# Kernel tuning notes

Hardware: AMD Instinct MI355X
Metric: run time of the kernel (lower is better)

The kernel has to match this reference:

```python
import jax, jax.numpy as jnp
import numpy as np

N_NODES = 100000
N_EDGES = 1600000
IN_DIM = 128
HID = 64
N_CLASSES = 40
NEG_SLOPE = 0.2


def setup_inputs() -> dict:
    key = jax.random.key(0)
    ks = jax.random.split(key, 12)
    s_in = 1.0 / np.sqrt(IN_DIM)
    s_h = 1.0 / np.sqrt(HID)
    return {
        "x": jax.random.normal(ks[0], (N_NODES, IN_DIM), dtype=jnp.float32),
        "edge_index": jax.random.randint(ks[1], (2, N_EDGES), 0, N_NODES, dtype=jnp.int64),
        "W0": jax.random.normal(ks[2], (IN_DIM, HID), dtype=jnp.float32) * s_in,
        "a_s0": jax.random.normal(ks[3], (HID,), dtype=jnp.float32) * s_h,
        "a_d0": jax.random.normal(ks[4], (HID,), dtype=jnp.float32) * s_h,
        "b0": jnp.zeros((HID,), dtype=jnp.float32),
        "W1": jax.random.normal(ks[5], (HID, HID), dtype=jnp.float32) * s_h,
        "a_s1": jax.random.normal(ks[6], (HID,), dtype=jnp.float32) * s_h,
        "a_d1": jax.random.normal(ks[7], (HID,), dtype=jnp.float32) * s_h,
        "b1": jnp.zeros((HID,), dtype=jnp.float32),
        "Wl": jax.random.normal(ks[8], (HID, N_CLASSES), dtype=jnp.float32) * s_h,
        "bl": jnp.zeros((N_CLASSES,), dtype=jnp.float32),
    }


def gat_conv(x, src, dst, W, a_s, a_d, b, n_nodes):
    # single-head GATConv (PyG default heads=1), self-loops already in src/dst
    h = x @ W                                  # [N, d]
    e = jax.nn.leaky_relu((h @ a_s)[src] + (h @ a_d)[dst], NEG_SLOPE)  # [E]
    # segment softmax over incoming edges of each dst node
    m = jax.ops.segment_max(e, dst, num_segments=n_nodes)
    p = jnp.exp(e - m[dst])
    denom = jax.ops.segment_sum(p, dst, num_segments=n_nodes)
    alpha = p / (denom[dst] + 1e-16)           # [E]
    out = jax.ops.segment_sum(alpha[:, None] * h[src], dst, num_segments=n_nodes)
    return out + b


def reference(x, edge_index, W0, a_s0, a_d0, b0, W1, a_s1, a_d1, b1, Wl, bl):
    n = x.shape[0]
    loop = jnp.arange(n, dtype=edge_index.dtype)
    src = jnp.concatenate([edge_index[0], loop])
    dst = jnp.concatenate([edge_index[1], loop])
    h = gat_conv(x, src, dst, W0, a_s0, a_d0, b0, n)
    h = jax.nn.elu(h)
    h = gat_conv(h, src, dst, W1, a_s1, a_d1, b1, n)
    h = jax.nn.elu(h)
    return h @ Wl + bl
```

## Files before the change

### kernel.cpp

```cpp
#include <hip/hip_runtime.h>
#include <math.h>

#define NEG_SLOPE 0.2f
#define CAP 256
#define BSH 9
#define BSZ 512
#define CHUNK 2048
#define PADS 16
#define HGRID 256

typedef __attribute__((ext_vector_type(8))) short short8;
typedef __attribute__((ext_vector_type(4))) float f32x4;

__device__ __forceinline__ float hred_sum(float v) {
#pragma unroll
    for (int o = 16; o >= 1; o >>= 1) v += __shfl_xor(v, o, 64);
    return v;
}
__device__ __forceinline__ unsigned int f2bf(float f) {
    unsigned int u = __float_as_uint(f);
    return (u + 0x7fffu + ((u >> 16) & 1u)) >> 16;
}
__device__ __forceinline__ float bflo(unsigned int u) { return __uint_as_float(u << 16); }
__device__ __forceinline__ float bfhi(unsigned int u) { return __uint_as_float(u & 0xffff0000u); }


__global__ __launch_bounds__(256) void k_hist(const int* __restrict__ dst, int* __restrict__ bpart, int E) {
    __shared__ int lh[256];
    lh[threadIdx.x] = 0;
    __syncthreads();
    int gid = blockIdx.x * 256 + threadIdx.x;
    int nth = gridDim.x * 256;
    int E4 = E >> 2;
    for (int i = gid; i < E4; i += nth) {
        int4 d = ((const int4*)dst)[i];
        atomicAdd(&lh[d.x >> BSH], 1);
        atomicAdd(&lh[d.y >> BSH], 1);
        atomicAdd(&lh[d.z >> BSH], 1);
        atomicAdd(&lh[d.w >> BSH], 1);
    }
    for (int i = (E4 << 2) + gid; i < E; i += nth)
        atomicAdd(&lh[dst[i] >> BSH], 1);
    __syncthreads();
    bpart[blockIdx.x * 256 + threadIdx.x] = lh[threadIdx.x];
}

__global__ __launch_bounds__(256) void k_bscan(const int* __restrict__ bpart,
                                               int* __restrict__ eoff, int* __restrict__ boff,
                                               int* __restrict__ bcursor, int* __restrict__ ecnt,
                                               int* __restrict__ rowptr,
                                               int nbuck, int N, int E) {
    __shared__ int s1[256], s2[256];
    int t = threadIdx.x;
    int bc = 0;
    for (int b = 0; b < HGRID; b += 4) {
        bc += bpart[(b + 0) * 256 + t];
        bc += bpart[(b + 1) * 256 + t];
        bc += bpart[(b + 2) * 256 + t];
        bc += bpart[(b + 3) * 256 + t];
    }
    if (t >= nbuck) bc = 0;
    int cn = 0;
    if (t < nbuck) { cn = N - (t << BSH); if (cn > BSZ) cn = BSZ; if (cn < 0) cn = 0; }
    int tot = bc + cn;
    s1[t] = bc; s2[t] = tot;
    __syncthreads();
#pragma unroll
    for (int off = 1; off < 256; off <<= 1) {
        int u1 = (t >= off) ? s1[t - off] : 0;
        int u2 = (t >= off) ? s2[t - off] : 0;
        __syncthreads();
        s1[t] += u1; s2[t] += u2;
        __syncthreads();
    }
    if (t < nbuck) {
        int e = s1[t] - bc, b = s2[t] - tot;
        eoff[t] = e; boff[t] = b; ecnt[t] = bc; bcursor[t * PADS] = e;
    }
    if (t == 0) rowptr[N] = E + N;
}


__device__ __forceinline__ void scatter_body(char* smem, int bid,
        const int* __restrict__ src, const int* __restrict__ dst,
        int* __restrict__ bcursor, int* __restrict__ ebuf, int E) {
    int* lh = (int*)smem;
    int* lb = lh + 256;
    const int tid = threadIdx.x;
    int base = bid * CHUNK;
    int sv[8], dv[8];
    bool ok[8];
#pragma unroll
    for (int u = 0; u < 8; ++u) {
        int i = base + u * 256 + tid;
        ok[u] = i < E;
        int ii = ok[u] ? i : E - 1;
        dv[u] = dst[ii];
        sv[u] = src[ii];
    }
    lh[tid] = 0;
    __syncthreads();
#pragma unroll
    for (int u = 0; u < 8; ++u)
        if (ok[u]) atomicAdd(&lh[dv[u] >> BSH], 1);
    __syncthreads();
    int c = lh[tid];
    lb[tid] = c ? atomicAdd(&bcursor[tid * PADS], c) : 0;
    lh[tid] = 0;
    __syncthreads();
#pragma unroll
    for (int u = 0; u < 8; ++u) {
        if (ok[u]) {
            int d = dv[u], b = d >> BSH;
            int pp = atomicAdd(&lh[b], 1);
            ebuf[lb[b] + pp] = (sv[u] << BSH) | (d & (BSZ - 1));
        }
    }
}

__device__ __forceinline__ void gemm0_body(char* smem, int bid,
        const float* __restrict__ X, const float* __restrict__ W,
        const float* __restrict__ a_s, const float* __restrict__ a_d,
        unsigned int* __restrict__ hb, float* __restrict__ ss, float* __restrict__ sd, int N) {
    constexpr int K = 128, OUTW = 64, NKC = K / 32, NC = OUTW / 16;
    short* wfrag = (short*)smem;
    unsigned int* hs = (unsigned int*)(smem + NKC * NC * 64 * 8 * 2);

    const int tid  = threadIdx.x;
    const int lane = tid & 63;
    const int w    = tid >> 6;
    const int m    = lane & 15;
    const int q8   = lane >> 4;
    const int rowbase = bid * 64 + w * 16;

    for (int f = tid; f < NKC * NC * 64; f += 256) {
        int flane = f & 63;
        int fc    = (f >> 6) % NC;
        int fkc   = (f >> 6) / NC;
        int col   = fc * 16 + (flane & 15);
        int k0    = fkc * 32 + (flane >> 4) * 8;
        short8 b;
#pragma unroll
        for (int j = 0; j < 8; ++j) b[j] = (short)f2bf(W[(k0 + j) * OUTW + col]);
        *(short8*)&wfrag[f * 8] = b;
    }
    __syncthreads();

    int grow = rowbase + m; if (grow >= N) grow = N - 1;

    f32x4 acc[NC];
#pragma unroll
    for (int c = 0; c < NC; ++c) acc[c] = (f32x4)0.f;

    const float* xrow = X + (size_t)grow * K + q8 * 8;
#pragma unroll
    for (int kc = 0; kc < NKC; ++kc) {
        float4 v0 = *(const float4*)(xrow + kc * 32);
        float4 v1 = *(const float4*)(xrow + kc * 32 + 4);
        float vv[8] = {v0.x, v0.y, v0.z, v0.w, v1.x, v1.y, v1.z, v1.w};
        short8 ah, al;
#pragma unroll
        for (int j = 0; j < 8; ++j) {
            unsigned int hb16 = f2bf(vv[j]);
            ah[j] = (short)hb16;
            al[j] = (short)f2bf(vv[j] - __uint_as_float(hb16 << 16));
        }
#pragma unroll
        for (int c = 0; c < NC; ++c) {
            short8 b = *(short8*)&wfrag[((kc * NC + c) * 64 + lane) * 8];
            acc[c] = __builtin_amdgcn_mfma_f32_16x16x32_bf16(ah, b, acc[c], 0, 0, 0);
            acc[c] = __builtin_amdgcn_mfma_f32_16x16x32_bf16(al, b, acc[c], 0, 0, 0);
        }
    }

    float asv[NC], adv[NC];
#pragma unroll
    for (int c = 0; c < NC; ++c) { asv[c] = a_s[c * 16 + m]; adv[c] = a_d[c * 16 + m]; }
#pragma unroll
    for (int i = 0; i < 4; ++i) {
        float s = 0.f, d = 0.f;
#pragma unroll
        for (int c = 0; c < NC; ++c) {
            s = fmaf(acc[c][i], asv[c], s);
            d = fmaf(acc[c][i], adv[c], d);
        }
#pragma unroll
        for (int o = 1; o <= 8; o <<= 1) {
            s += __shfl_xor(s, o, 64);
            d += __shfl_xor(d, o, 64);
        }
        int r = rowbase + q8 * 4 + i;
        if (m == 0 && r < N) { ss[r] = s; sd[r] = d; }
    }

    unsigned short* hsw = (unsigned short*)&hs[w * 512];
#pragma unroll
    for (int c = 0; c < NC; ++c)
#pragma unroll
        for (int i = 0; i < 4; ++i)
            hsw[(q8 * 4 + i) * 64 + c * 16 + m] = (unsigned short)f2bf(acc[c][i]);
    unsigned int* hu = &hs[w * 512];
    int row = lane >> 2, u0 = (lane & 3) * 8;
    uint4 va = *(uint4*)&hu[row * 32 + u0];
    uint4 vb = *(uint4*)&hu[row * 32 + u0 + 4];
    int r = rowbase + row;
    if (r < N) {
        *(uint4*)&hb[(size_t)r * 32 + u0]     = va;
        *(uint4*)&hb[(size_t)r * 32 + u0 + 4] = vb;
    }
}

__global__ __launch_bounds__(256) void k_scatter_gemm0(
        const int* __restrict__ src, const int* __restrict__ dst,
        int* __restrict__ bcursor, int* __restrict__ ebuf, int E, int nscat,
        const float* __restrict__ X, const float* __restrict__ W,
        const float* __restrict__ a_s, const float* __restrict__ a_d,
        unsigned int* __restrict__ hb, float* __restrict__ ss, float* __restrict__ sd, int N) {
    __shared__ __align__(16) char smem[24576];
    if ((int)blockIdx.x < nscat)
        scatter_body(smem, blockIdx.x, src, dst, bcursor, ebuf, E);
    else
        gemm0_body(smem, blockIdx.x - nscat, X, W, a_s, a_d, hb, ss, sd, N);
}

__global__ __launch_bounds__(512) void k_build(const int* __restrict__ eoff, const int* __restrict__ boff,
                                               const int* __restrict__ ecnt, const int* __restrict__ ebuf,
                                               int* __restrict__ rowptr, int* __restrict__ csr, int N) {
    __shared__ int sdeg[BSZ], sscan[BSZ];
    int b = blockIdx.x, t = threadIdx.x;
    int nlo = b << BSH;
    int cn = N - nlo; if (cn > BSZ) cn = BSZ;
    int e0 = eoff[b], ec = ecnt[b], cb = boff[b];
    sdeg[t] = (t < cn) ? 1 : 0;
    __syncthreads();
    {
        int i = t;
        for (; i + 1536 < ec; i += 2048) {
            int r0 = ebuf[e0 + i], r1 = ebuf[e0 + i + 512];
            int r2 = ebuf[e0 + i + 1024], r3 = ebuf[e0 + i + 1536];
            atomicAdd(&sdeg[r0 & (BSZ - 1)], 1);
            atomicAdd(&sdeg[r1 & (BSZ - 1)], 1);
            atomicAdd(&sdeg[r2 & (BSZ - 1)], 1);
            atomicAdd(&sdeg[r3 & (BSZ - 1)], 1);
        }
        for (; i < ec; i += 512)
            atomicAdd(&sdeg[ebuf[e0 + i] & (BSZ - 1)], 1);
    }
    __syncthreads();
    int v = sdeg[t];
    sscan[t] = v;
    __syncthreads();
#pragma unroll
    for (int off = 1; off < BSZ; off <<= 1) {
        int u = (t >= off) ? sscan[t - off] : 0;
        __syncthreads();
        sscan[t] += u;
        __syncthreads();
    }
    int excl = sscan[t] - v;
    if (t < cn) {
        rowptr[nlo + t] = cb + excl;
        csr[cb + excl] = nlo + t;
        sdeg[t] = excl + 1;
    }
    __syncthreads();
    {
        int i = t;
        for (; i + 1536 < ec; i += 2048) {
            int r0 = ebuf[e0 + i], r1 = ebuf[e0 + i + 512];
            int r2 = ebuf[e0 + i + 1024], r3 = ebuf[e0 + i + 1536];
            int p0 = atomicAdd(&sdeg[r0 & (BSZ - 1)], 1);
            int p1 = atomicAdd(&sdeg[r1 & (BSZ - 1)], 1);
            int p2 = atomicAdd(&sdeg[r2 & (BSZ - 1)], 1);
            int p3 = atomicAdd(&sdeg[r3 & (BSZ - 1)], 1);
            csr[cb + p0] = r0 >> BSH;
            csr[cb + p1] = r1 >> BSH;
            csr[cb + p2] = r2 >> BSH;
            csr[cb + p3] = r3 >> BSH;
        }
        for (; i < ec; i += 512) {
            int rec = ebuf[e0 + i];
            int p = atomicAdd(&sdeg[rec & (BSZ - 1)], 1);
            csr[cb + p] = rec >> BSH;
        }
    }
}


template <int K, int OUTW, bool SS, bool HB, bool XB>
__global__ __launch_bounds__(256) void k_gemm(const void* __restrict__ X,
                                              const float* __restrict__ W,
                                              const float* __restrict__ a_s,
                                              const float* __restrict__ a_d,
                                              const float* __restrict__ bias,
                                              void* __restrict__ Hout,
                                              float* __restrict__ ss,
                                              float* __restrict__ sd, int N) {
    constexpr int NKC = K / 32;
    constexpr int NC  = (OUTW + 15) / 16;
    __shared__ __align__(16) short wfrag[NKC * NC * 64 * 8];
    __shared__ __align__(16) unsigned int hs[HB ? 4 : 1][16 * 32];

    const int tid  = threadIdx.x;
    const int lane = tid & 63;
    const int w    = tid >> 6;
    const int m    = lane & 15;
    const int q8   = lane >> 4;
    const int rowbase = blockIdx.x * 64 + w * 16;

    for (int f = tid; f < NKC * NC * 64; f += 256) {
        int flane = f & 63;
        int fc    = (f >> 6) % NC;
        int fkc   = (f >> 6) / NC;
        int col   = fc * 16 + (flane & 15);
        int k0    = fkc * 32 + (flane >> 4) * 8;
        short8 b;
#pragma unroll
        for (int j = 0; j < 8; ++j) {
            float v = (col < OUTW) ? W[(k0 + j) * OUTW + col] : 0.f;
            b[j] = (short)f2bf(v);
        }
        *(short8*)&wfrag[f * 8] = b;
    }
    __syncthreads();

    int grow = rowbase + m; if (grow >= N) grow = N - 1;

    f32x4 acc[NC];
#pragma unroll
    for (int c = 0; c < NC; ++c) acc[c] = (f32x4)0.f;

    if (XB) {
        const unsigned short* xrow = (const unsigned short*)X + (size_t)grow * 64 + q8 * 8;
#pragma unroll
        for (int kc = 0; kc < NKC; ++kc) {
            short8 ah = *(const short8*)(xrow + kc * 32);
#pragma unroll
            for (int c = 0; c < NC; ++c) {
                short8 b = *(short8*)&wfrag[((kc * NC + c) * 64 + lane) * 8];
                acc[c] = __builtin_amdgcn_mfma_f32_16x16x32_bf16(ah, b, acc[c], 0, 0, 0);
            }
        }
    } else {
        const float* xrow = (const float*)X + (size_t)grow * K + q8 * 8;
#pragma unroll
        for (int kc = 0; kc < NKC; ++kc) {
            float4 v0 = *(const float4*)(xrow + kc * 32);
            float4 v1 = *(const float4*)(xrow + kc * 32 + 4);
            float vv[8] = {v0.x, v0.y, v0.z, v0.w, v1.x, v1.y, v1.z, v1.w};
            short8 ah, al;
#pragma unroll
            for (int j = 0; j < 8; ++j) {
                unsigned int hb16 = f2bf(vv[j]);
                ah[j] = (short)hb16;
                al[j] = (short)f2bf(vv[j] - __uint_as_float(hb16 << 16));
            }
#pragma unroll
            for (int c = 0; c < NC; ++c) {
                short8 b = *(short8*)&wfrag[((kc * NC + c) * 64 + lane) * 8];
                acc[c] = __builtin_amdgcn_mfma_f32_16x16x32_bf16(ah, b, acc[c], 0, 0, 0);
                acc[c] = __builtin_amdgcn_mfma_f32_16x16x32_bf16(al, b, acc[c], 0, 0, 0);
            }
        }
    }

    if (SS) {
        float asv[NC], adv[NC];
#pragma unroll
        for (int c = 0; c < NC; ++c) { asv[c] = a_s[c * 16 + m]; adv[c] = a_d[c * 16 + m]; }
#pragma unroll
        for (int i = 0; i < 4; ++i) {
            float s = 0.f, d = 0.f;
#pragma unroll
            for (int c = 0; c < NC; ++c) {
                s = fmaf(acc[c][i], asv[c], s);
                d = fmaf(acc[c][i], adv[c], d);
            }
#pragma unroll
            for (int o = 1; o <= 8; o <<= 1) {
                s += __shfl_xor(s, o, 64);
                d += __shfl_xor(d, o, 64);
            }
            int r = rowbase + q8 * 4 + i;
            if (m == 0 && r < N) { ss[r] = s; sd[r] = d; }
        }
    }

    if (HB) {
        unsigned short* hsw = (unsigned short*)&hs[w][0];
#pragma unroll
        for (int c = 0; c < NC; ++c)
#pragma unroll
            for (int i = 0; i < 4; ++i)
                hsw[(q8 * 4 + i) * 64 + c * 16 + m] = (unsigned short)f2bf(acc[c][i]);
        unsigned int* hu = &hs[w][0];
        int row = lane >> 2, u0 = (lane & 3) * 8;
        uint4 va = *(uint4*)&hu[row * 32 + u0];
        uint4 vb = *(uint4*)&hu[row * 32 + u0 + 4];
        int r = rowbase + row;
        if (r < N) {
            unsigned int* hbp = (unsigned int*)Hout;
            *(uint4*)&hbp[(size_t)r * 32 + u0]     = va;
            *(uint4*)&hbp[(size_t)r * 32 + u0 + 4] = vb;
        }
    } else {
        float bv[NC];
#pragma unroll
        for (int c = 0; c < NC; ++c) {
            int col = c * 16 + m;
            bv[c] = (col < OUTW) ? bias[col] : 0.f;
        }
        float* O = (float*)Hout;
#pragma unroll
        for (int i = 0; i < 4; ++i) {
            int r = rowbase + q8 * 4 + i;
            if (r < N) {
#pragma unroll
                for (int c = 0; c < NC; ++c) {
                    int col = c * 16 + m;
                    if (col < OUTW) O[(size_t)r * OUTW + col] = acc[c][i] + bv[c];
                }
            }
        }
    }
}


__global__ __launch_bounds__(256) void k_agg(const int* __restrict__ rowptr, const int* __restrict__ csr,
                                             const float* __restrict__ ss, const float* __restrict__ sd,
                                             const unsigned int* __restrict__ hb, const float* __restrict__ bias,
                                             unsigned int* __restrict__ z, int N) {
    __shared__ __align__(16) float sal[8][CAP];
    __shared__ __align__(16) int   sof[8][CAP];
    const int tid = threadIdx.x;
    const int hw  = tid >> 5;
    const int p   = tid & 31;
    const int n   = blockIdx.x * 8 + hw;
    const bool valid = n < N;
    const char* hbb = (const char*)hb;
    const int p4 = p * 4;

    int ro = 0, deg = 0;
    float sdn = 0.f;
    if (valid) {
        ro  = rowptr[n];
        deg = rowptr[n + 1] - ro;
        sdn = sd[n];
    }

    if (deg <= CAP) {
        float sum = 0.f;
        for (int j = p; j < deg; j += 32) {
            int s = csr[ro + j];
            float e = ss[s] + sdn;
            e = fmaxf(e, NEG_SLOPE * e);
            float pe = __expf(e);
            sal[hw][j] = pe;
            sof[hw][j] = s << 7;
            sum += pe;
        }
        sum = hred_sum(sum);
        float inv = 1.f / (sum + 1e-16f);

        float ax = 0.f, ay = 0.f, bx = 0.f, by = 0.f, cx = 0.f, cy = 0.f, dx = 0.f, dy = 0.f;
        int j = 0;
        for (; j + 7 < deg; j += 8) {
            float4 al0 = *(const float4*)&sal[hw][j];
            float4 al1 = *(const float4*)&sal[hw][j + 4];
            int4   of0 = *(const int4*)&sof[hw][j];
            int4   of1 = *(const int4*)&sof[hw][j + 4];
            unsigned int u0 = *(const unsigned int*)(hbb + (of0.x + p4));
            unsigned int u1 = *(const unsigned int*)(hbb + (of0.y + p4));
            unsigned int u2 = *(const unsigned int*)(hbb + (of0.z + p4));
            unsigned int u3 = *(const unsigned int*)(hbb + (of0.w + p4));
            unsigned int u4 = *(const unsigned int*)(hbb + (of1.x + p4));
            unsigned int u5 = *(const unsigned int*)(hbb + (of1.y + p4));
            unsigned int u6 = *(const unsigned int*)(hbb + (of1.z + p4));
            unsigned int u7 = *(const unsigned int*)(hbb + (of1.w + p4));
            ax = fmaf(bflo(u0), al0.x, ax); ay = fmaf(bfhi(u0), al0.x, ay);
            bx = fmaf(bflo(u1), al0.y, bx); by = fmaf(bfhi(u1), al0.y, by);
            cx = fmaf(bflo(u2), al0.z, cx); cy = fmaf(bfhi(u2), al0.z, cy);
            dx = fmaf(bflo(u3), al0.w, dx); dy = fmaf(bfhi(u3), al0.w, dy);
            ax = fmaf(bflo(u4), al1.x, ax); ay = fmaf(bfhi(u4), al1.x, ay);
            bx = fmaf(bflo(u5), al1.y, bx); by = fmaf(bfhi(u5), al1.y, by);
            cx = fmaf(bflo(u6), al1.z, cx); cy = fmaf(bfhi(u6), al1.z, cy);
            dx = fmaf(bflo(u7), al1.w, dx); dy = fmaf(bfhi(u7), al1.w, dy);
        }
        for (; j + 3 < deg; j += 4) {
            float4 al0 = *(const float4*)&sal[hw][j];
            int4   of0 = *(const int4*)&sof[hw][j];
            unsigned int u0 = *(const unsigned int*)(hbb + (of0.x + p4));
            unsigned int u1 = *(const unsigned int*)(hbb + (of0.y + p4));
            unsigned int u2 = *(const unsigned int*)(hbb + (of0.z + p4));
            unsigned int u3 = *(const unsigned int*)(hbb + (of0.w + p4));
            ax = fmaf(bflo(u0), al0.x, ax); ay = fmaf(bfhi(u0), al0.x, ay);
            bx = fmaf(bflo(u1), al0.y, bx); by = fmaf(bfhi(u1), al0.y, by);
            cx = fmaf(bflo(u2), al0.z, cx); cy = fmaf(bfhi(u2), al0.z, cy);
            dx = fmaf(bflo(u3), al0.w, dx); dy = fmaf(bfhi(u3), al0.w, dy);
        }
        for (; j < deg; ++j) {
            float a = sal[hw][j];
            unsigned int u0 = *(const unsigned int*)(hbb + (sof[hw][j] + p4));
            ax = fmaf(bflo(u0), a, ax); ay = fmaf(bfhi(u0), a, ay);
        }
        float fx = (ax + bx) + (cx + dx);
        float fy = (ay + by) + (cy + dy);
        if (valid) {
            float2 ob = *(const float2*)&bias[p * 2];
            float ox = fmaf(fx, inv, ob.x);
            float oy = fmaf(fy, inv, ob.y);
            ox = (ox > 0.f) ? ox : __expf(ox) - 1.f;
            oy = (oy > 0.f) ? oy : __expf(oy) - 1.f;
            z[(size_t)n * 32 + p] = (f2bf(oy) << 16) | f2bf(ox);
        }
    } else {
        float sum = 0.f;
        for (int j = p; j < deg; j += 32) {
            int s = csr[ro + j];
            float e = ss[s] + sdn;
            e = fmaxf(e, NEG_SLOPE * e);
            sum += __expf(e);
        }
        sum = hred_sum(sum);
        float inv = 1.f / (sum + 1e-16f);
        float fx = 0.f, fy = 0.f;
        for (int j = 0; j < deg; ++j) {
            int s = csr[ro + j];
            float e = ss[s] + sdn;
            e = fmaxf(e, NEG_SLOPE * e);
            float pe = __expf(e);
            unsigned int u = *(const unsigned int*)(hbb + ((s << 7) + p4));
            fx = fmaf(bflo(u), pe, fx); fy = fmaf(bfhi(u), pe, fy);
        }
        float2 ob = *(const float2*)&bias[p * 2];
        float ox = fmaf(fx, inv, ob.x);
        float oy = fmaf(fy, inv, ob.y);
        ox = (ox > 0.f) ? ox : __expf(ox) - 1.f;
        oy = (oy > 0.f) ? oy : __expf(oy) - 1.f;
        z[(size_t)n * 32 + p] = (f2bf(oy) << 16) | f2bf(ox);
    }
}


extern "C" void kernel_launch(void* const* d_in, const int* in_sizes, int n_in,
                              void* d_out, int out_size, void* d_ws, size_t ws_size,
                              hipStream_t stream) {
    const float* x   = (const float*)d_in[0];
    const int*   ei  = (const int*)d_in[1];
    const float* W0  = (const float*)d_in[2];
    const float* as0 = (const float*)d_in[3];
    const float* ad0 = (const float*)d_in[4];
    const float* b0  = (const float*)d_in[5];
    const float* W1  = (const float*)d_in[6];
    const float* as1 = (const float*)d_in[7];
    const float* ad1 = (const float*)d_in[8];
    const float* b1  = (const float*)d_in[9];
    const float* Wl  = (const float*)d_in[10];
    const float* bl  = (const float*)d_in[11];
    float* out = (float*)d_out;

    int N = in_sizes[0] / 128;
    int E = in_sizes[1] / 2;
    const int* srcp = ei;
    const int* dstp = ei + E;
    int nbuck = (N + BSZ - 1) >> BSH;

    char* wp = (char*)d_ws;
    auto alloc = [&](size_t bytes) { void* p = (void*)wp; wp += (bytes + 255) & ~(size_t)255; return p; };
    unsigned int* hb = (unsigned int*)alloc((size_t)N * 32 * 4);
    unsigned int* z  = (unsigned int*)alloc((size_t)N * 32 * 4);
    float* ssb     = (float*)alloc((size_t)N * 4);
    float* sdb     = (float*)alloc((size_t)N * 4);
    int*   rowptr  = (int*)alloc((size_t)(N + 1) * 4);
    int*   csr     = (int*)alloc((size_t)(E + N) * 4);
    int*   ebuf    = (int*)alloc((size_t)E * 4);
    int*   bpart   = (int*)alloc((size_t)HGRID * 256 * 4);
    int*   eoff    = (int*)alloc(256 * 4);
    int*   boff    = (int*)alloc(256 * 4);
    int*   ecnt    = (int*)alloc(256 * 4);
    int*   bcursor = (int*)alloc(256 * PADS * 4);

    int nscat = (E + CHUNK - 1) / CHUNK;
    int gb = (N + 63) / 64;

    k_hist<<<HGRID, 256, 0, stream>>>(dstp, bpart, E);
    k_bscan<<<1, 256, 0, stream>>>(bpart, eoff, boff, bcursor, ecnt, rowptr, nbuck, N, E);
    k_scatter_gemm0<<<nscat + gb, 256, 0, stream>>>(srcp, dstp, bcursor, ebuf, E, nscat,
                                                    x, W0, as0, ad0, hb, ssb, sdb, N);
    k_build<<<nbuck, 512, 0, stream>>>(eoff, boff, ecnt, ebuf, rowptr, csr, N);

    k_agg<<<(N + 7) / 8, 256, 0, stream>>>(rowptr, csr, ssb, sdb, hb, b0, z, N);
    k_gemm<64, 64, true, true, true><<<gb, 256, 0, stream>>>(z, W1, as1, ad1, nullptr, hb, ssb, sdb, N);
    k_agg<<<(N + 7) / 8, 256, 0, stream>>>(rowptr, csr, ssb, sdb, hb, b1, z, N);
    k_gemm<64, 40, false, false, true><<<gb, 256, 0, stream>>>(z, Wl, nullptr, nullptr, bl, out, nullptr, nullptr, N);
}
```

Baseline: 264.0 us.

## Cache bucket edges in LDS during CSR build, widen build blocks and scatter chunks

The CSR build kernel now stages each bucket's edge records in a 40KB shared-memory buffer on the first pass and reads them back from LDS on the second pass, instead of reading ebuf from global memory twice. The build block grows from 512 to 1024 threads, with the degree scan guarded to the first 512 threads. The scatter phase processes 4096 edges per block instead of 2048, which halves the number of scatter blocks and the global cursor atomics. The costs are a larger LDS footprint that limits occupancy, and a global fallback path for buckets with more than CAPB edges.

```diff
diff --git a/kernel.cpp b/kernel.cpp
--- a/kernel.cpp
+++ b/kernel.cpp
@@ -5,9 +5,10 @@
 #define CAP 256
 #define BSH 9
 #define BSZ 512
-#define CHUNK 2048
+#define CHUNK 4096
 #define PADS 16
 #define HGRID 256
+#define CAPB 10240
 
 typedef __attribute__((ext_vector_type(8))) short short8;
 typedef __attribute__((ext_vector_type(4))) float f32x4;
@@ -88,10 +89,10 @@
     int* lb = lh + 256;
     const int tid = threadIdx.x;
     int base = bid * CHUNK;
-    int sv[8], dv[8];
-    bool ok[8];
-#pragma unroll
-    for (int u = 0; u < 8; ++u) {
+    int sv[16], dv[16];
+    bool ok[16];
+#pragma unroll
+    for (int u = 0; u < 16; ++u) {
         int i = base + u * 256 + tid;
         ok[u] = i < E;
         int ii = ok[u] ? i : E - 1;
@@ -101,7 +102,7 @@
     lh[tid] = 0;
     __syncthreads();
 #pragma unroll
-    for (int u = 0; u < 8; ++u)
+    for (int u = 0; u < 16; ++u)
         if (ok[u]) atomicAdd(&lh[dv[u] >> BSH], 1);
     __syncthreads();
     int c = lh[tid];
@@ -109,7 +110,7 @@
     lh[tid] = 0;
     __syncthreads();
 #pragma unroll
-    for (int u = 0; u < 8; ++u) {
+    for (int u = 0; u < 16; ++u) {
         if (ok[u]) {
             int d = dv[u], b = d >> BSH;
             int pp = atomicAdd(&lh[b], 1);
@@ -223,52 +224,64 @@
         gemm0_body(smem, blockIdx.x - nscat, X, W, a_s, a_d, hb, ss, sd, N);
 }
 
-__global__ __launch_bounds__(512) void k_build(const int* __restrict__ eoff, const int* __restrict__ boff,
-                                               const int* __restrict__ ecnt, const int* __restrict__ ebuf,
-                                               int* __restrict__ rowptr, int* __restrict__ csr, int N) {
+
+__global__ __launch_bounds__(1024) void k_build(const int* __restrict__ eoff, const int* __restrict__ boff,
+                                                const int* __restrict__ ecnt, const int* __restrict__ ebuf,
+                                                int* __restrict__ rowptr, int* __restrict__ csr, int N) {
     __shared__ int sdeg[BSZ], sscan[BSZ];
+    __shared__ int sebuf[CAPB];
     int b = blockIdx.x, t = threadIdx.x;
     int nlo = b << BSH;
     int cn = N - nlo; if (cn > BSZ) cn = BSZ;
     int e0 = eoff[b], ec = ecnt[b], cb = boff[b];
-    sdeg[t] = (t < cn) ? 1 : 0;
-    __syncthreads();
+    if (t < BSZ) sdeg[t] = (t < cn) ? 1 : 0;
+    __syncthreads();
+    int ecl = ec < CAPB ? ec : CAPB;
     {
         int i = t;
-        for (; i + 1536 < ec; i += 2048) {
-            int r0 = ebuf[e0 + i], r1 = ebuf[e0 + i + 512];
-            int r2 = ebuf[e0 + i + 1024], r3 = ebuf[e0 + i + 1536];
+        for (; i + 3 * 1024 < ecl; i += 4 * 1024) {
+            int r0 = ebuf[e0 + i],        r1 = ebuf[e0 + i + 1024];
+            int r2 = ebuf[e0 + i + 2048], r3 = ebuf[e0 + i + 3072];
+            sebuf[i] = r0; sebuf[i + 1024] = r1; sebuf[i + 2048] = r2; sebuf[i + 3072] = r3;
             atomicAdd(&sdeg[r0 & (BSZ - 1)], 1);
             atomicAdd(&sdeg[r1 & (BSZ - 1)], 1);
             atomicAdd(&sdeg[r2 & (BSZ - 1)], 1);
             atomicAdd(&sdeg[r3 & (BSZ - 1)], 1);
         }
-        for (; i < ec; i += 512)
+        for (; i < ecl; i += 1024) {
+            int r = ebuf[e0 + i];
+            sebuf[i] = r;
+            atomicAdd(&sdeg[r & (BSZ - 1)], 1);
+        }
+        for (i = CAPB + t; i < ec; i += 1024)
             atomicAdd(&sdeg[ebuf[e0 + i] & (BSZ - 1)], 1);
     }
     __syncthreads();
-    int v = sdeg[t];
-    sscan[t] = v;
+    int v = 0;
+    if (t < BSZ) { v = sdeg[t]; sscan[t] = v; }
     __syncthreads();
 #pragma unroll
     for (int off = 1; off < BSZ; off <<= 1) {
-        int u = (t >= off) ? sscan[t - off] : 0;
+        int u = 0;
+        if (t < BSZ && t >= off) u = sscan[t - off];
         __syncthreads();
-        sscan[t] += u;
+        if (t < BSZ) sscan[t] += u;
         __syncthreads();
     }
-    int excl = sscan[t] - v;
-    if (t < cn) {
-        rowptr[nlo + t] = cb + excl;
-        csr[cb + excl] = nlo + t;
-        sdeg[t] = excl + 1;
+    if (t < BSZ) {
+        int excl = sscan[t] - v;
+        if (t < cn) {
+            rowptr[nlo + t] = cb + excl;
+            csr[cb + excl] = nlo + t;
+            sdeg[t] = excl + 1;
+        }
     }
     __syncthreads();
     {
         int i = t;
-        for (; i + 1536 < ec; i += 2048) {
-            int r0 = ebuf[e0 + i], r1 = ebuf[e0 + i + 512];
-            int r2 = ebuf[e0 + i + 1024], r3 = ebuf[e0 + i + 1536];
+        for (; i + 3 * 1024 < ecl; i += 4 * 1024) {
+            int r0 = sebuf[i],        r1 = sebuf[i + 1024];
+            int r2 = sebuf[i + 2048], r3 = sebuf[i + 3072];
             int p0 = atomicAdd(&sdeg[r0 & (BSZ - 1)], 1);
             int p1 = atomicAdd(&sdeg[r1 & (BSZ - 1)], 1);
             int p2 = atomicAdd(&sdeg[r2 & (BSZ - 1)], 1);
@@ -278,7 +291,12 @@
             csr[cb + p2] = r2 >> BSH;
             csr[cb + p3] = r3 >> BSH;
         }
-        for (; i < ec; i += 512) {
+        for (; i < ecl; i += 1024) {
+            int rec = sebuf[i];
+            int p = atomicAdd(&sdeg[rec & (BSZ - 1)], 1);
+            csr[cb + p] = rec >> BSH;
+        }
+        for (i = CAPB + t; i < ec; i += 1024) {
             int rec = ebuf[e0 + i];
             int p = atomicAdd(&sdeg[rec & (BSZ - 1)], 1);
             csr[cb + p] = rec >> BSH;
@@ -587,7 +605,7 @@
     k_bscan<<<1, 256, 0, stream>>>(bpart, eoff, boff, bcursor, ecnt, rowptr, nbuck, N, E);
     k_scatter_gemm0<<<nscat + gb, 256, 0, stream>>>(srcp, dstp, bcursor, ebuf, E, nscat,
                                                     x, W0, as0, ad0, hb, ssb, sdb, N);
-    k_build<<<nbuck, 512, 0, stream>>>(eoff, boff, ecnt, ebuf, rowptr, csr, N);
+    k_build<<<nbuck, 1024, 0, stream>>>(eoff, boff, ecnt, ebuf, rowptr, csr, N);
 
     k_agg<<<(N + 7) / 8, 256, 0, stream>>>(rowptr, csr, ssb, sdb, hb, b0, z, N);
     k_gemm<64, 64, true, true, true><<<gb, 256, 0, stream>>>(z, W1, as1, ad1, nullptr, hb, ssb, sdb, N);
```

New measurement: 253.3 us. 1.04x faster.
